# Kernel tuning notes

Hardware: AMD Instinct MI355X
Metric: run time of the kernel (lower is better)

Reference implementation:

```python
import jax, jax.numpy as jnp
import numpy as np

EPS = 1e-8

def _penalty(v, lo, hi):
    # if v<lo: (lo-v)/lo ; elif v>hi (hi finite): (v-hi)/hi ; else 0
    below = (lo - v) / lo
    if np.isinf(hi):
        return jnp.where(v < lo, below, 0.0)
    above = (v - hi) / hi
    return jnp.where(v < lo, below, jnp.where(v > hi, above, 0.0))

def _symbolic_features(x):
    # x: [B, input_dim]; column mapping from the original per-row loop
    am, bod, do, ph, nit = x[:, 0], x[:, 1], x[:, 2], x[:, 4], x[:, 7]
    # penalties in param_order = [ph, ammonia, bod, dissolved_oxygen, nitrate]
    p_ph  = _penalty(ph, 6.5, 8.5)
    p_am  = _penalty(am, 0.001, 0.5)
    p_bod = _penalty(bod, 0.001, 5.0)
    p_do  = _penalty(do, 6.0, np.inf)
    p_nit = _penalty(nit, 0.001, 10.0)
    # pollutant scores (missing params like 'nitrogen'/'orthophosphate' are skipped -> count adjusts)
    s_bact = (1.2 * am / (0.5 + EPS) + 1.5 * bod / (5.0 + EPS) - 0.8 * do / (10.0 + EPS)) / 3.0
    s_chem = (1.5 * ph / (8.5 + EPS) + 1.0 * nit / (10.0 + EPS)) / 2.0
    s_org  = (2.0 * bod / (5.0 + EPS) - 1.5 * do / (10.0 + EPS) + 0.8 * am / (0.5 + EPS)) / 3.0
    s_agr  = (2.0 * nit / (10.0 + EPS)) / 1.0
    resil = 1.0 / (1.0 + (p_ph + p_am + p_bod + p_do + p_nit) + EPS)
    return jnp.stack([p_ph, p_am, p_bod, p_do, p_nit, s_bact, s_chem, s_org, s_agr, resil], axis=1)

def setup_inputs() -> dict:
    key = jax.random.key(0)
    ks = jax.random.split(key, 16)
    B, D_IN, SYM, H = 1048576, 10, 10, 64
    def lin(k, fin, fout):
        k1, k2 = jax.random.split(k)
        s = 1.0 / np.sqrt(fin)
        return (jax.random.uniform(k1, (fin, fout), jnp.float32, -s, s),
                jax.random.uniform(k2, (fout,), jnp.float32, -s, s))
    W_sym, b_sym = lin(ks[0], SYM, H // 2)
    W_in, b_in = lin(ks[1], D_IN + H // 2, H)
    W1, b1 = lin(ks[2], H, H)
    W2, b2 = lin(ks[3], H, H)
    W3, b3 = lin(ks[4], H, H)
    W_r1, b_r1 = lin(ks[5], H, H // 2)
    W_r2, b_r2 = lin(ks[6], H // 2, 1)
    W_c1, b_c1 = lin(ks[7], H, H // 2)
    W_c2, b_c2 = lin(ks[8], H // 2, 4)
    x = jax.random.uniform(ks[9], (B, D_IN), jnp.float32)
    return {"x": x, "W_sym": W_sym, "b_sym": b_sym, "W_in": W_in, "b_in": b_in,
            "W1": W1, "b1": b1, "W2": W2, "b2": b2, "W3": W3, "b3": b3,
            "W_r1": W_r1, "b_r1": b_r1, "W_r2": W_r2, "b_r2": b_r2,
            "W_c1": W_c1, "b_c1": b_c1, "W_c2": W_c2, "b_c2": b_c2}

def reference(x, W_sym, b_sym, W_in, b_in, W1, b1, W2, b2, W3, b3,
              W_r1, b_r1, W_r2, b_r2, W_c1, b_c1, W_c2, b_c2):
    elu = jax.nn.elu
    sym = _symbolic_features(x)                      # [B, 10]
    sym_enc = elu(sym @ W_sym + b_sym)               # [B, 32]  (Dropout: eval mode = identity)
    h = elu(jnp.concatenate([x, sym_enc], axis=1) @ W_in + b_in)  # [B, 64]
    for W, b in ((W1, b1), (W2, b2), (W3, b3)):
        h = h + elu(h @ W + b)                       # residual MLP stack
    predictions = elu(h @ W_r1 + b_r1) @ W_r2 + b_r2            # [B, 1]
    pollutant_logits = elu(h @ W_c1 + b_c1) @ W_c2 + b_c2       # [B, 4]
    return predictions, pollutant_logits
```

## Files before the change

### kernel.cpp

```cpp
#include <hip/hip_runtime.h>
#include <hip/hip_bf16.h>
#include <math.h>

#define NROWS 1048576
#define EPSF 1e-8f

typedef unsigned short ushortT;
typedef __attribute__((ext_vector_type(8))) short short8;
typedef __attribute__((ext_vector_type(4))) float floatx4;

#define WS_HI   256
#define WS_LO   41216
#define WS_MF   82176
#define MF_B5   0
#define MF_WSYM 320
#define MF_BSYM 640
#define MF_WR2  672
#define MF_BR2  704
#define MF_WC2  708
#define MF_BC2  836

#define LDS_FENCE() asm volatile("s_waitcnt lgkmcnt(0)" ::: "memory")

struct WPtrs { const void* p[19]; };

__global__ void sniff_kernel(const ushortT* __restrict__ x, int* __restrict__ flag) {
    if (threadIdx.x == 0 && blockIdx.x == 0) {
        unsigned s = 0;
        for (int i = 0; i < 64; ++i) s |= (unsigned)(x[i] & 0x8000u);
        *flag = s ? 1 : 0;
    }
}

__device__ __forceinline__ float ldw(const void* p, int i, bool f32) {
    return f32 ? ((const float*)p)[i]
               : __uint_as_float(((unsigned)((const ushortT*)p)[i]) << 16);
}

__global__ void prep_kernel(WPtrs wp, const int* __restrict__ flag, void* __restrict__ ws) {
    const bool f32 = (*flag != 0);
    ushortT* hi = (ushortT*)((char*)ws + WS_HI);
    ushortT* lo = (ushortT*)((char*)ws + WS_LO);
    float* mf = (float*)((char*)ws + WS_MF);
    const int B = blockIdx.x;
    if (B < 5) {
        for (int idx = threadIdx.x; idx < 4096; idx += 256) {
            const int j = idx & 7, ln = (idx >> 3) & 63, t = (idx >> 9) & 3, s = idx >> 11;
            const int k = s * 32 + (ln >> 4) * 8 + j;
            const int n = t * 16 + (ln & 15);
            float w = 0.0f;
            if (B == 0)      { if (k < 42) w = ldw(wp.p[3], k * 64 + n, f32); }
            else if (B <= 3) { w = ldw(wp.p[3 + 2 * B], k * 64 + n, f32); }
            else             { w = (n < 32) ? ldw(wp.p[11], k * 32 + n, f32)
                                            : ldw(wp.p[15], k * 32 + (n - 32), f32); }
            const unsigned u = __float_as_uint(w);
            const float rem = w - __uint_as_float(u & 0xffff0000u);
            hi[B * 4096 + idx] = (ushortT)(u >> 16);
            lo[B * 4096 + idx] = (ushortT)(__float_as_uint(rem) >> 16);
        }
    } else {
        const int src[12] = {4, 6, 8, 10, 12, 16, 1, 2, 13, 14, 17, 18};
        const int cnt[12] = {64, 64, 64, 64, 32, 32, 320, 32, 32, 1, 128, 4};
        const int dst[12] = {0, 64, 128, 192, 256, 288, MF_WSYM, MF_BSYM, MF_WR2, MF_BR2, MF_WC2, MF_BC2};
        for (int a = 0; a < 12; ++a)
            for (int i = threadIdx.x; i < cnt[a]; i += 256)
                mf[dst[a] + i] = ldw(wp.p[src[a]], i, f32);
    }
}

__device__ __forceinline__ float eluf(float v) {
    return v > 0.0f ? v : __expf(v) - 1.0f;
}
__device__ __forceinline__ float pen2(float v, float lo, float hi) {
    return v < lo ? (lo - v) / lo : (v > hi ? (v - hi) / hi : 0.0f);
}
__device__ __forceinline__ float pen1(float v, float lo) {
    return v < lo ? (lo - v) / lo : 0.0f;
}

__global__ __launch_bounds__(256, 4) void mlp_mfma_kernel(
    const void* __restrict__ xin, const int* __restrict__ flagp,
    const void* __restrict__ ws, void* __restrict__ out)
{
    const ushortT* __restrict__ wfhi = (const ushortT*)((const char*)ws + WS_HI);
    const ushortT* __restrict__ wflo = (const ushortT*)((const char*)ws + WS_LO);
    const float* __restrict__ mf = (const float*)((const char*)ws + WS_MF);

    __shared__ float hball[4][16][68];
    const int tid = threadIdx.x;
    const int wave = tid >> 6, lane = tid & 63;
    float (* __restrict__ hb)[68] = hball[wave];
    const int m = lane & 15, q = lane >> 4;
    const bool isf32 = (*flagp != 0);
    const int rowg = blockIdx.x * 64 + wave * 16 + m;

    #pragma unroll
    for (int it = 0; it < 6; ++it) {
        const int i = lane + (it << 6);
        if (i < 352) hb[i & 15][42 + (i >> 4)] = 0.0f;
    }

    float x[10];
    if (isf32) {
        const float* xp = (const float*)xin + (size_t)rowg * 10;
        #pragma unroll
        for (int i = 0; i < 10; ++i) x[i] = xp[i];
    } else {
        const ushortT* xp = (const ushortT*)xin + (size_t)rowg * 10;
        #pragma unroll
        for (int i = 0; i < 10; ++i) x[i] = __uint_as_float(((unsigned)xp[i]) << 16);
    }
    if (q == 0) {
        #pragma unroll
        for (int i = 0; i < 10; ++i) hb[m][i] = x[i];
    }

    const float am = x[0], bod = x[1], dox = x[2], ph = x[4], nit = x[7];
    const float p_ph  = pen2(ph, 6.5f, 8.5f);
    const float p_am  = pen2(am, 0.001f, 0.5f);
    const float p_bod = pen2(bod, 0.001f, 5.0f);
    const float p_do  = pen1(dox, 6.0f);
    const float p_nit = pen2(nit, 0.001f, 10.0f);
    const float s_bact = (1.2f * am / (0.5f + EPSF) + 1.5f * bod / (5.0f + EPSF)
                          - 0.8f * dox / (10.0f + EPSF)) / 3.0f;
    const float s_chem = (1.5f * ph / (8.5f + EPSF) + 1.0f * nit / (10.0f + EPSF)) / 2.0f;
    const float s_org  = (2.0f * bod / (5.0f + EPSF) - 1.5f * dox / (10.0f + EPSF)
                          + 0.8f * am / (0.5f + EPSF)) / 3.0f;
    const float s_agr  = 2.0f * nit / (10.0f + EPSF);
    const float resil  = 1.0f / (1.0f + (p_ph + p_am + p_bod + p_do + p_nit) + EPSF);
    const float sym[10] = {p_ph, p_am, p_bod, p_do, p_nit, s_bact, s_chem, s_org, s_agr, resil};

    float se[8];
    #pragma unroll
    for (int jj = 0; jj < 8; ++jj) se[jj] = mf[MF_BSYM + q * 8 + jj];
    #pragma unroll
    for (int k = 0; k < 10; ++k) {
        #pragma unroll
        for (int jj = 0; jj < 8; ++jj)
            se[jj] = fmaf(sym[k], mf[MF_WSYM + k * 32 + q * 8 + jj], se[jj]);
    }
    #pragma unroll
    for (int jj = 0; jj < 8; ++jj) hb[m][10 + q * 8 + jj] = eluf(se[jj]);
    LDS_FENCE();

    floatx4 acc[4];
    #pragma unroll
    for (int L = 0; L < 5; ++L) {
        #pragma unroll
        for (int t = 0; t < 4; ++t) {
            const float b = mf[MF_B5 + L * 64 + t * 16 + m];
            acc[t] = (floatx4){b, b, b, b};
        }
        #pragma unroll
        for (int s = 0; s < 2; ++s) {
            const floatx4 f0 = *(const floatx4*)&hb[m][s * 32 + q * 8];
            const floatx4 f1 = *(const floatx4*)&hb[m][s * 32 + q * 8 + 4];
            short8 ahi, alo;
            #pragma unroll
            for (int i = 0; i < 8; ++i) {
                const float fv = (i < 4) ? f0[i] : f1[i - 4];
                const unsigned u = __float_as_uint(fv);
                ahi[i] = (short)(u >> 16);
                const float r = fv - __uint_as_float(u & 0xffff0000u);
                alo[i] = (short)(__float_as_uint(r) >> 16);
            }
            const int tbase = (L * 2 + s) << 2;
            #pragma unroll
            for (int t = 0; t < 4; ++t) {
                const short8 bh = *(const short8*)(wfhi + (size_t)((tbase + t) << 9) + lane * 8);
                acc[t] = __builtin_amdgcn_mfma_f32_16x16x32_bf16(ahi, bh, acc[t], 0, 0, 0);
                acc[t] = __builtin_amdgcn_mfma_f32_16x16x32_bf16(alo, bh, acc[t], 0, 0, 0);
                if (isf32) {
                    const short8 bl = *(const short8*)(wflo + (size_t)((tbase + t) << 9) + lane * 8);
                    acc[t] = __builtin_amdgcn_mfma_f32_16x16x32_bf16(ahi, bl, acc[t], 0, 0, 0);
                }
            }
        }
        LDS_FENCE();
        #pragma unroll
        for (int t = 0; t < 4; ++t) {
            #pragma unroll
            for (int r = 0; r < 4; ++r) {
                float e = eluf(acc[t][r]);
                const int rr = (q << 2) + r, cc = (t << 4) + m;
                if (L >= 1 && L <= 3) e += hb[rr][cc];
                hb[rr][cc] = e;
            }
        }
        LDS_FENCE();
    }

    float accp = mf[MF_BR2];
    float accl = mf[MF_BC2 + q];
    #pragma unroll
    for (int j = 0; j < 32; ++j) {
        accp = fmaf(hb[m][j],      mf[MF_WR2 + j],         accp);
        accl = fmaf(hb[m][32 + j], mf[MF_WC2 + j * 4 + q], accl);
    }
    if (isf32) {
        float* o = (float*)out;
        if (q == 0) o[rowg] = accp;
        o[NROWS + rowg * 4 + q] = accl;
    } else {
        __hip_bfloat16* o = (__hip_bfloat16*)out;
        if (q == 0) o[rowg] = __float2bfloat16(accp);
        o[NROWS + rowg * 4 + q] = __float2bfloat16(accl);
    }
}

extern "C" void kernel_launch(void* const* d_in, const int* in_sizes, int n_in,
                              void* d_out, int out_size, void* d_ws, size_t ws_size,
                              hipStream_t stream) {
    (void)in_sizes; (void)n_in; (void)out_size; (void)ws_size;
    int* flag = (int*)d_ws;

    sniff_kernel<<<1, 64, 0, stream>>>((const ushortT*)d_in[0], flag);

    WPtrs wp;
    for (int i = 0; i < 19; ++i) wp.p[i] = d_in[i];
    prep_kernel<<<6, 256, 0, stream>>>(wp, flag, d_ws);

    mlp_mfma_kernel<<<NROWS / 64, 256, 0, stream>>>(d_in[0], flag, d_ws, d_out);
}
```

Measured before the change: 350.9 us.

## Template kernel on input precision and micro-optimize split, ELU, penalties and epilogue

Splits the kernel body into a template specialized on fp32 versus bf16 input, so the per-MFMA runtime branch disappears. Other edits: packs the hi/lo bf16 split with perm instructions, makes ELU branchless, replaces the penalty divisions with constant reciprocals, and preloads all biases into registers. It also keeps the residual hidden state in registers instead of re-reading LDS, vectorizes the symbolic-encoder and head loads, and transposes the classifier weight so those reads can be vector loads. The specialization doubles code size, and the reciprocal constants can differ slightly in rounding from the reference divisions.

```diff
diff --git a/kernel.cpp b/kernel.cpp
--- a/kernel.cpp
+++ b/kernel.cpp
@@ -8,6 +8,7 @@
 typedef unsigned short ushortT;
 typedef __attribute__((ext_vector_type(8))) short short8;
 typedef __attribute__((ext_vector_type(4))) float floatx4;
+typedef __attribute__((ext_vector_type(4))) int intx4;
 
 #define WS_HI   256
 #define WS_LO   41216
@@ -19,6 +20,7 @@
 #define MF_BR2  704
 #define MF_WC2  708
 #define MF_BC2  836
+#define MF_WC2T 840
 
 #define LDS_FENCE() asm volatile("s_waitcnt lgkmcnt(0)" ::: "memory")
 
@@ -65,34 +67,50 @@
         for (int a = 0; a < 12; ++a)
             for (int i = threadIdx.x; i < cnt[a]; i += 256)
                 mf[dst[a] + i] = ldw(wp.p[src[a]], i, f32);
+        for (int i = threadIdx.x; i < 128; i += 256) {
+            const int qq = i >> 5, j = i & 31;
+            mf[MF_WC2T + i] = ldw(wp.p[17], j * 4 + qq, f32);
+        }
     }
 }
 
 __device__ __forceinline__ float eluf(float v) {
-    return v > 0.0f ? v : __expf(v) - 1.0f;
-}
-__device__ __forceinline__ float pen2(float v, float lo, float hi) {
-    return v < lo ? (lo - v) / lo : (v > hi ? (v - hi) / hi : 0.0f);
-}
-__device__ __forceinline__ float pen1(float v, float lo) {
-    return v < lo ? (lo - v) / lo : 0.0f;
-}
-
-__global__ __launch_bounds__(256, 4) void mlp_mfma_kernel(
-    const void* __restrict__ xin, const int* __restrict__ flagp,
-    const void* __restrict__ ws, void* __restrict__ out)
+    return fmaxf(v, 0.0f) + (__expf(fminf(v, 0.0f)) - 1.0f);
+}
+
+__device__ __forceinline__ unsigned pack_hi16(unsigned ua, unsigned ub) {
+    return __builtin_amdgcn_perm(ub, ua, 0x07060302u);
+}
+
+__device__ __forceinline__ void split8(const floatx4 f0, const floatx4 f1,
+                                       short8& ahi, short8& alo) {
+    float fv[8];
+    #pragma unroll
+    for (int i = 0; i < 4; ++i) { fv[i] = f0[i]; fv[4 + i] = f1[i]; }
+    intx4 hi_i, lo_i;
+    #pragma unroll
+    for (int d = 0; d < 4; ++d) {
+        const float a = fv[2 * d], b = fv[2 * d + 1];
+        const unsigned ua = __float_as_uint(a), ub = __float_as_uint(b);
+        hi_i[d] = (int)pack_hi16(ua, ub);
+        const float la = a - __uint_as_float(ua & 0xffff0000u);
+        const float lb = b - __uint_as_float(ub & 0xffff0000u);
+        lo_i[d] = (int)pack_hi16(__float_as_uint(la), __float_as_uint(lb));
+    }
+    ahi = __builtin_bit_cast(short8, hi_i);
+    alo = __builtin_bit_cast(short8, lo_i);
+}
+
+template<bool F32>
+__device__ __forceinline__ void run_body(
+    const void* __restrict__ xin, const char* __restrict__ wsb,
+    void* __restrict__ out, float (* __restrict__ hb)[68],
+    const int lane, const int rowg)
 {
-    const ushortT* __restrict__ wfhi = (const ushortT*)((const char*)ws + WS_HI);
-    const ushortT* __restrict__ wflo = (const ushortT*)((const char*)ws + WS_LO);
-    const float* __restrict__ mf = (const float*)((const char*)ws + WS_MF);
-
-    __shared__ float hball[4][16][68];
-    const int tid = threadIdx.x;
-    const int wave = tid >> 6, lane = tid & 63;
-    float (* __restrict__ hb)[68] = hball[wave];
+    const ushortT* __restrict__ wfhi = (const ushortT*)(wsb + WS_HI);
+    const ushortT* __restrict__ wflo = (const ushortT*)(wsb + WS_LO);
+    const float* __restrict__ mf = (const float*)(wsb + WS_MF);
     const int m = lane & 15, q = lane >> 4;
-    const bool isf32 = (*flagp != 0);
-    const int rowg = blockIdx.x * 64 + wave * 16 + m;
 
     #pragma unroll
     for (int it = 0; it < 6; ++it) {
@@ -100,15 +118,26 @@
         if (i < 352) hb[i & 15][42 + (i >> 4)] = 0.0f;
     }
 
+    float bias[5][4];
+    #pragma unroll
+    for (int L = 0; L < 5; ++L)
+        #pragma unroll
+        for (int t = 0; t < 4; ++t)
+            bias[L][t] = mf[MF_B5 + L * 64 + t * 16 + m];
+
     float x[10];
-    if (isf32) {
+    if (F32) {
         const float* xp = (const float*)xin + (size_t)rowg * 10;
         #pragma unroll
         for (int i = 0; i < 10; ++i) x[i] = xp[i];
     } else {
-        const ushortT* xp = (const ushortT*)xin + (size_t)rowg * 10;
-        #pragma unroll
-        for (int i = 0; i < 10; ++i) x[i] = __uint_as_float(((unsigned)xp[i]) << 16);
+        const unsigned* xd = (const unsigned*)((const ushortT*)xin + (size_t)rowg * 10);
+        #pragma unroll
+        for (int i = 0; i < 5; ++i) {
+            const unsigned d = xd[i];
+            x[2 * i]     = __uint_as_float(d << 16);
+            x[2 * i + 1] = __uint_as_float(d & 0xffff0000u);
+        }
     }
     if (q == 0) {
         #pragma unroll
@@ -116,39 +145,50 @@
     }
 
     const float am = x[0], bod = x[1], dox = x[2], ph = x[4], nit = x[7];
-    const float p_ph  = pen2(ph, 6.5f, 8.5f);
-    const float p_am  = pen2(am, 0.001f, 0.5f);
-    const float p_bod = pen2(bod, 0.001f, 5.0f);
-    const float p_do  = pen1(dox, 6.0f);
-    const float p_nit = pen2(nit, 0.001f, 10.0f);
-    const float s_bact = (1.2f * am / (0.5f + EPSF) + 1.5f * bod / (5.0f + EPSF)
-                          - 0.8f * dox / (10.0f + EPSF)) / 3.0f;
-    const float s_chem = (1.5f * ph / (8.5f + EPSF) + 1.0f * nit / (10.0f + EPSF)) / 2.0f;
-    const float s_org  = (2.0f * bod / (5.0f + EPSF) - 1.5f * dox / (10.0f + EPSF)
-                          + 0.8f * am / (0.5f + EPSF)) / 3.0f;
-    const float s_agr  = 2.0f * nit / (10.0f + EPSF);
+    const float p_ph  = ph  < 6.5f   ? (6.5f - ph) * 0.15384616f
+                      : (ph > 8.5f   ? (ph - 8.5f) * 0.11764706f : 0.0f);
+    const float p_am  = am  < 0.001f ? (0.001f - am) * 1000.0f
+                      : (am > 0.5f   ? (am - 0.5f) * 2.0f : 0.0f);
+    const float p_bod = bod < 0.001f ? (0.001f - bod) * 1000.0f
+                      : (bod > 5.0f  ? (bod - 5.0f) * 0.2f : 0.0f);
+    const float p_do  = dox < 6.0f   ? (6.0f - dox) * 0.16666667f : 0.0f;
+    const float p_nit = nit < 0.001f ? (0.001f - nit) * 1000.0f
+                      : (nit > 10.0f ? (nit - 10.0f) * 0.1f : 0.0f);
+    const float s_bact = (am * 2.3999999f + bod * 0.29999998f - dox * 0.08f) * 0.33333334f;
+    const float s_chem = (ph * 0.17647059f + nit * 0.1f) * 0.5f;
+    const float s_org  = (bod * 0.39999998f - dox * 0.14999999f + am * 1.5999999f) * 0.33333334f;
+    const float s_agr  = nit * 0.2f;
     const float resil  = 1.0f / (1.0f + (p_ph + p_am + p_bod + p_do + p_nit) + EPSF);
     const float sym[10] = {p_ph, p_am, p_bod, p_do, p_nit, s_bact, s_chem, s_org, s_agr, resil};
 
     float se[8];
-    #pragma unroll
-    for (int jj = 0; jj < 8; ++jj) se[jj] = mf[MF_BSYM + q * 8 + jj];
-    #pragma unroll
-    for (int k = 0; k < 10; ++k) {
-        #pragma unroll
-        for (int jj = 0; jj < 8; ++jj)
-            se[jj] = fmaf(sym[k], mf[MF_WSYM + k * 32 + q * 8 + jj], se[jj]);
+    {
+        const floatx4 b0 = *(const floatx4*)(mf + MF_BSYM + q * 8);
+        const floatx4 b1 = *(const floatx4*)(mf + MF_BSYM + q * 8 + 4);
+        #pragma unroll
+        for (int jj = 0; jj < 4; ++jj) { se[jj] = b0[jj]; se[4 + jj] = b1[jj]; }
+        #pragma unroll
+        for (int k = 0; k < 10; ++k) {
+            const floatx4 w0 = *(const floatx4*)(mf + MF_WSYM + k * 32 + q * 8);
+            const floatx4 w1 = *(const floatx4*)(mf + MF_WSYM + k * 32 + q * 8 + 4);
+            #pragma unroll
+            for (int jj = 0; jj < 4; ++jj) {
+                se[jj]     = fmaf(sym[k], w0[jj], se[jj]);
+                se[4 + jj] = fmaf(sym[k], w1[jj], se[4 + jj]);
+            }
+        }
     }
     #pragma unroll
     for (int jj = 0; jj < 8; ++jj) hb[m][10 + q * 8 + jj] = eluf(se[jj]);
     LDS_FENCE();
 
-    floatx4 acc[4];
+    floatx4 hcd[4];
     #pragma unroll
     for (int L = 0; L < 5; ++L) {
+        floatx4 acc[4];
         #pragma unroll
         for (int t = 0; t < 4; ++t) {
-            const float b = mf[MF_B5 + L * 64 + t * 16 + m];
+            const float b = bias[L][t];
             acc[t] = (floatx4){b, b, b, b};
         }
         #pragma unroll
@@ -156,35 +196,27 @@
             const floatx4 f0 = *(const floatx4*)&hb[m][s * 32 + q * 8];
             const floatx4 f1 = *(const floatx4*)&hb[m][s * 32 + q * 8 + 4];
             short8 ahi, alo;
-            #pragma unroll
-            for (int i = 0; i < 8; ++i) {
-                const float fv = (i < 4) ? f0[i] : f1[i - 4];
-                const unsigned u = __float_as_uint(fv);
-                ahi[i] = (short)(u >> 16);
-                const float r = fv - __uint_as_float(u & 0xffff0000u);
-                alo[i] = (short)(__float_as_uint(r) >> 16);
-            }
+            split8(f0, f1, ahi, alo);
             const int tbase = (L * 2 + s) << 2;
             #pragma unroll
             for (int t = 0; t < 4; ++t) {
                 const short8 bh = *(const short8*)(wfhi + (size_t)((tbase + t) << 9) + lane * 8);
                 acc[t] = __builtin_amdgcn_mfma_f32_16x16x32_bf16(ahi, bh, acc[t], 0, 0, 0);
                 acc[t] = __builtin_amdgcn_mfma_f32_16x16x32_bf16(alo, bh, acc[t], 0, 0, 0);
-                if (isf32) {
+                if (F32) {
                     const short8 bl = *(const short8*)(wflo + (size_t)((tbase + t) << 9) + lane * 8);
                     acc[t] = __builtin_amdgcn_mfma_f32_16x16x32_bf16(ahi, bl, acc[t], 0, 0, 0);
                 }
             }
         }
-        LDS_FENCE();
         #pragma unroll
         for (int t = 0; t < 4; ++t) {
             #pragma unroll
             for (int r = 0; r < 4; ++r) {
-                float e = eluf(acc[t][r]);
-                const int rr = (q << 2) + r, cc = (t << 4) + m;
-                if (L >= 1 && L <= 3) e += hb[rr][cc];
-                hb[rr][cc] = e;
+                const float e = eluf(acc[t][r]);
+                const float h = (L >= 1 && L <= 3) ? hcd[t][r] + e : e;
+                hcd[t][r] = h;
+                hb[(q << 2) + r][(t << 4) + m] = h;
             }
         }
         LDS_FENCE();
@@ -192,12 +224,20 @@
 
     float accp = mf[MF_BR2];
     float accl = mf[MF_BC2 + q];
-    #pragma unroll
-    for (int j = 0; j < 32; ++j) {
-        accp = fmaf(hb[m][j],      mf[MF_WR2 + j],         accp);
-        accl = fmaf(hb[m][32 + j], mf[MF_WC2 + j * 4 + q], accl);
-    }
-    if (isf32) {
+    const float* wct = mf + MF_WC2T + q * 32;
+    #pragma unroll
+    for (int jj = 0; jj < 8; ++jj) {
+        const floatx4 hv = *(const floatx4*)&hb[m][jj * 4];
+        const floatx4 hw = *(const floatx4*)&hb[m][32 + jj * 4];
+        const floatx4 wc = *(const floatx4*)&wct[jj * 4];
+        #pragma unroll
+        for (int r = 0; r < 4; ++r) {
+            accp = fmaf(hv[r], mf[MF_WR2 + jj * 4 + r], accp);
+            accl = fmaf(hw[r], wc[r], accl);
+        }
+    }
+
+    if (F32) {
         float* o = (float*)out;
         if (q == 0) o[rowg] = accp;
         o[NROWS + rowg * 4 + q] = accl;
@@ -208,6 +248,20 @@
     }
 }
 
+__global__ __launch_bounds__(256, 4) void mlp_mfma_kernel(
+    const void* __restrict__ xin, const int* __restrict__ flagp,
+    const void* __restrict__ ws, void* __restrict__ out)
+{
+    __shared__ float hball[4][16][68];
+    const int tid = threadIdx.x;
+    const int wave = tid >> 6, lane = tid & 63;
+    const int rowg = blockIdx.x * 64 + wave * 16 + (lane & 15);
+    if (*flagp != 0)
+        run_body<true>(xin, (const char*)ws, out, hball[wave], lane, rowg);
+    else
+        run_body<false>(xin, (const char*)ws, out, hball[wave], lane, rowg);
+}
+
 extern "C" void kernel_launch(void* const* d_in, const int* in_sizes, int n_in,
                               void* d_out, int out_size, void* d_ws, size_t ws_size,
                               hipStream_t stream) {
```

Result: no change. 347.4 us (-1.0%).
